# Kernel tuning notes

Measured on AMD Instinct MI355X. Metric: run time of the kernel, lower is better.

## Reference

```python
import jax, jax.numpy as jnp
import numpy as np

N_NODES = 50000
N_EDGES = 800000
N_GRAPHS = 256
NEG_SLOPE = 0.2

def selu(x):
    return jax.nn.selu(x)

def gat_conv(x, src, dst, W, att_l, att_r, b, n_nodes):
    """PyG GATConv, heads=1, with self-loops already appended to (src, dst).
    Message j->i: alpha_ij = softmax_i(leaky_relu(a_l.h_j + a_r.h_i)); out_i = sum_j alpha_ij h_j + b."""
    h = x @ W                                   # [N, C]
    a_src = h @ att_l                           # [N]
    a_dst = h @ att_r                           # [N]
    e = jax.nn.leaky_relu(a_src[src] + a_dst[dst], NEG_SLOPE)   # [E]
    # segment softmax over incoming edges of each dst node
    m = jax.ops.segment_max(e, dst, num_segments=n_nodes)       # [N]
    m = jnp.where(jnp.isfinite(m), m, 0.0)
    ex = jnp.exp(e - m[dst])
    denom = jax.ops.segment_sum(ex, dst, num_segments=n_nodes)  # [N]
    alpha = ex / jnp.maximum(denom, 1e-16)[dst]                  # [E]
    out = jax.ops.segment_sum(h[src] * alpha[:, None], dst, num_segments=n_nodes)
    return out + b

def global_mean_pool(x, batch, n_graphs):
    s = jax.ops.segment_sum(x, batch, num_segments=n_graphs)
    cnt = jax.ops.segment_sum(jnp.ones((x.shape[0],), x.dtype), batch, num_segments=n_graphs)
    return s / jnp.maximum(cnt, 1.0)[:, None]

def setup_inputs() -> dict:
    key = jax.random.key(0)
    ks = jax.random.split(key, 12)
    F_in, C, H, NC = 310, 256, 128, 2
    x = jax.random.normal(ks[0], (N_NODES, F_in), dtype=jnp.float32)
    edge_index = jax.random.randint(ks[1], (2, N_EDGES), 0, N_NODES, dtype=jnp.int64)
    batch = jnp.sort(jax.random.randint(ks[2], (N_NODES,), 0, N_GRAPHS, dtype=jnp.int64))
    g = lambda k, shp: jax.random.normal(k, shp, dtype=jnp.float32) * 0.05
    return {
        "x": x, "edge_index": edge_index, "batch": batch,
        "W1": g(ks[3], (F_in, C)), "att_l1": g(ks[4], (C,)), "att_r1": g(ks[5], (C,)),
        "b1": jnp.zeros((C,), jnp.float32),
        "W2": g(ks[6], (C, C)), "att_l2": g(ks[7], (C,)), "att_r2": g(ks[8], (C,)),
        "b2": jnp.zeros((C,), jnp.float32),
        "fc1_W": g(ks[9], (C, H)), "fc1_b": jnp.zeros((H,), jnp.float32),
        "fc2_W": g(ks[10], (H, NC)), "fc2_b": jnp.zeros((NC,), jnp.float32),
    }

def reference(x, edge_index, batch, W1, att_l1, att_r1, b1, W2, att_l2, att_r2, b2,
              fc1_W, fc1_b, fc2_W, fc2_b):
    n = x.shape[0]
    loops = jnp.arange(n, dtype=edge_index.dtype)
    src = jnp.concatenate([edge_index[0], loops])   # add_self_loops=True (PyG default)
    dst = jnp.concatenate([edge_index[1], loops])
    h = selu(gat_conv(x, src, dst, W1, att_l1, att_r1, b1, n))
    h = selu(gat_conv(h, src, dst, W2, att_l2, att_r2, b2, n))
    g = selu(global_mean_pool(h, batch, N_GRAPHS))      # [G, 256]
    g = selu(g @ fc1_W + fc1_b)                         # [G, 128]
    # dropout is identity in eval mode
    return jax.nn.log_softmax(g @ fc2_W + fc2_b, axis=-1)  # [G, 2]
```

## Files before the change

### kernel.cpp

```cpp
#include <hip/hip_runtime.h>
#include <hip/hip_bf16.h>

#define N_NODES 50000
#define N_EDGES 800000
#define N_TOT   (N_EDGES + N_NODES)
#define N_GRAPHS 256
#define F_IN 310
#define KP1 320
#define CH 256
#define HID 128
#define DEG_CAP 128

typedef __attribute__((ext_vector_type(8))) short short8;
typedef __attribute__((ext_vector_type(4))) float f32x4;
typedef unsigned short ushort_t;

__device__ __forceinline__ float selu_f(float x) {
    const float scale = 1.0507009873554805f;
    const float alpha = 1.6732632423543772f;
    return x > 0.f ? scale * x : scale * alpha * (expm1f(x));
}

__device__ __forceinline__ ushort_t f32_to_bf16_rne(float f) {
    unsigned u = __float_as_uint(f);
    unsigned rounding = 0x7FFFu + ((u >> 16) & 1u);
    return (ushort_t)((u + rounding) >> 16);
}
__device__ __forceinline__ float bf16_to_f32(ushort_t v) {
    return __uint_as_float(((unsigned)v) << 16);
}

__global__ __launch_bounds__(256) void convert_pad_x(
        const float* __restrict__ x, ushort_t* __restrict__ A) {
    int i = blockIdx.x * 256 + threadIdx.x;
    if (i >= N_NODES * (KP1 / 2)) return;
    int r = i / (KP1 / 2);
    int c2 = i - r * (KP1 / 2);
    int c = c2 * 2;
    ushort2 o = {0, 0};
    if (c2 < F_IN / 2) {
        float2 v = *(const float2*)(x + (long)r * F_IN + c);
        o.x = f32_to_bf16_rne(v.x);
        o.y = f32_to_bf16_rne(v.y);
    }
    *(ushort2*)(A + (long)r * KP1 + c) = o;
}

__global__ __launch_bounds__(256) void convert_wt_both(
        const float* __restrict__ W1, ushort_t* __restrict__ W1t,
        const float* __restrict__ W2, ushort_t* __restrict__ W2t) {
    int i = blockIdx.x * blockDim.x + threadIdx.x;
    const int n1 = CH * KP1;
    if (i < n1) {
        int n = i / KP1, k = i % KP1;
        W1t[i] = (k < F_IN) ? f32_to_bf16_rne(W1[(long)k * CH + n]) : 0;
    } else {
        int j = i - n1;
        if (j >= CH * CH) return;
        int n = j / CH, k = j % CH;
        W2t[j] = f32_to_bf16_rne(W2[(long)k * CH + n]);
    }
}

__global__ __launch_bounds__(256) void gemm_bf16_fused(
        const ushort_t* __restrict__ A, const ushort_t* __restrict__ Bt,
        ushort_t* __restrict__ Cb, const float* __restrict__ att_l,
        const float* __restrict__ att_r, float* __restrict__ a_src,
        float* __restrict__ a_dst, int M, int Kp) {
    __shared__ __align__(16) ushort_t As[2][64 * 32];
    __shared__ __align__(16) ushort_t Bs[2][256 * 32];
    __shared__ float s_pl[64], s_pr[64];
    int tid = threadIdx.x;
    int row0 = blockIdx.x * 64;
    int w = tid >> 6, l = tid & 63;
    int lr = l & 15, lc = l >> 4;
    f32x4 acc[4][4] = {};

    int srow = l >> 2;
    int sx = (l & 3) ^ (srow & 3);
    int garow = row0 + w * 16 + srow; if (garow >= M) garow = M - 1;
    const ushort_t* gA = A + (size_t)garow * Kp + sx * 8;
    const ushort_t* gB[4];
#pragma unroll
    for (int g = 0; g < 4; ++g)
        gB[g] = Bt + (size_t)(w * 64 + g * 16 + srow) * Kp + sx * 8;
    int nt = Kp >> 5;

    auto stage = [&](int sel, int k0) {
        __builtin_amdgcn_global_load_lds(
            (const __attribute__((address_space(1))) void*)(gA + k0),
            (__attribute__((address_space(3))) void*)(&As[sel][w * 16 * 32]), 16, 0, 0);
#pragma unroll
        for (int g = 0; g < 4; ++g)
            __builtin_amdgcn_global_load_lds(
                (const __attribute__((address_space(1))) void*)(gB[g] + k0),
                (__attribute__((address_space(3))) void*)(&Bs[sel][(w * 64 + g * 16) * 32]), 16, 0, 0);
    };

    stage(0, 0);
    __syncthreads();
    int cur = 0;
    for (int t = 0; t < nt; ++t) {
        if (t + 1 < nt) stage(cur ^ 1, (t + 1) << 5);
        short8 af[4], bf[4];
#pragma unroll
        for (int mi = 0; mi < 4; ++mi) {
            int r = mi * 16 + lr;
            af[mi] = *(const short8*)(&As[cur][r * 32 + ((lc ^ (r & 3)) * 8)]);
        }
#pragma unroll
        for (int ni = 0; ni < 4; ++ni) {
            int r = w * 64 + ni * 16 + lr;
            bf[ni] = *(const short8*)(&Bs[cur][r * 32 + ((lc ^ (r & 3)) * 8)]);
        }
#pragma unroll
        for (int mi = 0; mi < 4; ++mi)
#pragma unroll
            for (int ni = 0; ni < 4; ++ni)
                acc[mi][ni] = __builtin_amdgcn_mfma_f32_16x16x32_bf16(
                    af[mi], bf[ni], acc[mi][ni], 0, 0, 0);
        __syncthreads();
        cur ^= 1;
    }

    if (tid < 64) { s_pl[tid] = 0.f; s_pr[tid] = 0.f; }
    __syncthreads();
    float al[4], ar[4];
#pragma unroll
    for (int ni = 0; ni < 4; ++ni) {
        int col = w * 64 + ni * 16 + lr;
        al[ni] = att_l[col];
        ar[ni] = att_r[col];
    }
#pragma unroll
    for (int mi = 0; mi < 4; ++mi) {
        int lrow = mi * 16 + lc * 4;
#pragma unroll
        for (int q = 0; q < 4; ++q) {
            int grow = row0 + lrow + q;
            float pl = 0.f, pr = 0.f;
#pragma unroll
            for (int ni = 0; ni < 4; ++ni) {
                float v = acc[mi][ni][q];
                pl += v * al[ni];
                pr += v * ar[ni];
                if (grow < M)
                    Cb[(size_t)grow * CH + w * 64 + ni * 16 + lr] = f32_to_bf16_rne(v);
            }
#pragma unroll
            for (int off = 1; off < 16; off <<= 1) {
                pl += __shfl_xor(pl, off);
                pr += __shfl_xor(pr, off);
            }
            if (lr == 0) {
                atomicAdd(&s_pl[lrow + q], pl);
                atomicAdd(&s_pr[lrow + q], pr);
            }
        }
    }
    __syncthreads();
    if (tid < 64 && row0 + tid < M) {
        a_src[row0 + tid] = s_pl[tid];
        a_dst[row0 + tid] = s_pr[tid];
    }
}

__global__ __launch_bounds__(256) void deg_count(
        const int* __restrict__ ei, int* __restrict__ deg) {
    int eid = blockIdx.x * blockDim.x + threadIdx.x;
    if (eid >= N_TOT) return;
    int d = (eid < N_EDGES) ? ei[N_EDGES + eid] : eid - N_EDGES;
    atomicAdd(&deg[d], 1);
}

__global__ __launch_bounds__(256) void reserve_k(
        const int* __restrict__ deg, int* __restrict__ start,
        int* __restrict__ fillpos, int* __restrict__ cursor, int n) {
    int i = blockIdx.x * blockDim.x + threadIdx.x;
    if (i >= n) return;
    int s = atomicAdd(cursor, deg[i]);
    start[i] = s;
    fillpos[i] = s;
}

__global__ __launch_bounds__(256) void csr_fill(
        const int* __restrict__ ei, int* __restrict__ fillpos,
        int* __restrict__ csr_src) {
    int eid = blockIdx.x * blockDim.x + threadIdx.x;
    if (eid >= N_TOT) return;
    int s, d;
    if (eid < N_EDGES) { s = ei[eid]; d = ei[N_EDGES + eid]; }
    else { s = eid - N_EDGES; d = s; }
    int p = atomicAdd(&fillpos[d], 1);
    csr_src[p] = s;
}

__global__ __launch_bounds__(256) void gat_aggregate(
        const int* __restrict__ start, const int* __restrict__ deg,
        const int* __restrict__ csr_src,
        const float* __restrict__ a_src, const float* __restrict__ a_dst,
        const ushort_t* __restrict__ h, const float* __restrict__ bias,
        ushort_t* __restrict__ out_bf, int n) {
    __shared__ int   s_idx[4][DEG_CAP];
    __shared__ float s_ex[4][DEG_CAP];
    int wid = threadIdx.x >> 6;
    int lane = threadIdx.x & 63;
    int node = blockIdx.x * 4 + wid;
    if (node >= n) return;
    int s0 = start[node];
    int dg = deg[node];
    float ad = a_dst[node];
    bool cached = (dg <= DEG_CAP);

    float sum = 0.f;
    for (int i = lane; i < dg; i += 64) {
        int s = csr_src[s0 + i];
        float e = a_src[s] + ad;
        e = fmaxf(e, 0.2f * e);
        float ex = __expf(e);
        if (cached) { s_idx[wid][i] = s; s_ex[wid][i] = ex; }
        sum += ex;
    }
#pragma unroll
    for (int off = 32; off > 0; off >>= 1) sum += __shfl_xor(sum, off);
    float inv = 1.f / fmaxf(sum, 1e-16f);

    float4 acc = {0.f, 0.f, 0.f, 0.f};
    if (cached) {
        int i = 0;
        for (; i + 8 <= dg; i += 8) {
            int   si[8];
            float xi[8];
            ushort4 hv[8];
#pragma unroll
            for (int j = 0; j < 8; ++j) {
                si[j] = s_idx[wid][i + j];
                xi[j] = s_ex[wid][i + j] * inv;
            }
#pragma unroll
            for (int j = 0; j < 8; ++j)
                hv[j] = *(const ushort4*)(h + (long)si[j] * CH + lane * 4);
#pragma unroll
            for (int j = 0; j < 8; ++j) {
                acc.x += xi[j] * bf16_to_f32(hv[j].x);
                acc.y += xi[j] * bf16_to_f32(hv[j].y);
                acc.z += xi[j] * bf16_to_f32(hv[j].z);
                acc.w += xi[j] * bf16_to_f32(hv[j].w);
            }
        }
        for (; i + 4 <= dg; i += 4) {
            int sa = s_idx[wid][i],     sb = s_idx[wid][i + 1];
            int sc_ = s_idx[wid][i + 2], sd = s_idx[wid][i + 3];
            float xa = s_ex[wid][i] * inv,     xb = s_ex[wid][i + 1] * inv;
            float xc = s_ex[wid][i + 2] * inv, xd = s_ex[wid][i + 3] * inv;
            ushort4 ha = *(const ushort4*)(h + (long)sa * CH + lane * 4);
            ushort4 hb = *(const ushort4*)(h + (long)sb * CH + lane * 4);
            ushort4 hc = *(const ushort4*)(h + (long)sc_ * CH + lane * 4);
            ushort4 hd = *(const ushort4*)(h + (long)sd * CH + lane * 4);
            acc.x += xa * bf16_to_f32(ha.x) + xb * bf16_to_f32(hb.x)
                   + xc * bf16_to_f32(hc.x) + xd * bf16_to_f32(hd.x);
            acc.y += xa * bf16_to_f32(ha.y) + xb * bf16_to_f32(hb.y)
                   + xc * bf16_to_f32(hc.y) + xd * bf16_to_f32(hd.y);
            acc.z += xa * bf16_to_f32(ha.z) + xb * bf16_to_f32(hb.z)
                   + xc * bf16_to_f32(hc.z) + xd * bf16_to_f32(hd.z);
            acc.w += xa * bf16_to_f32(ha.w) + xb * bf16_to_f32(hb.w)
                   + xc * bf16_to_f32(hc.w) + xd * bf16_to_f32(hd.w);
        }
        for (; i < dg; i++) {
            int s = s_idx[wid][i];
            float xa = s_ex[wid][i] * inv;
            ushort4 hv = *(const ushort4*)(h + (long)s * CH + lane * 4);
            acc.x += xa * bf16_to_f32(hv.x);
            acc.y += xa * bf16_to_f32(hv.y);
            acc.z += xa * bf16_to_f32(hv.z);
            acc.w += xa * bf16_to_f32(hv.w);
        }
    } else {
        for (int i = 0; i < dg; i++) {
            int s = csr_src[s0 + i];
            float e = a_src[s] + ad;
            e = fmaxf(e, 0.2f * e);
            float alpha = __expf(e) * inv;
            ushort4 hv = *(const ushort4*)(h + (long)s * CH + lane * 4);
            acc.x += alpha * bf16_to_f32(hv.x);
            acc.y += alpha * bf16_to_f32(hv.y);
            acc.z += alpha * bf16_to_f32(hv.z);
            acc.w += alpha * bf16_to_f32(hv.w);
        }
    }
    float4 bv = *(const float4*)(bias + lane * 4);
    ushort4 ob;
    ob.x = f32_to_bf16_rne(selu_f(acc.x + bv.x));
    ob.y = f32_to_bf16_rne(selu_f(acc.y + bv.y));
    ob.z = f32_to_bf16_rne(selu_f(acc.z + bv.z));
    ob.w = f32_to_bf16_rne(selu_f(acc.w + bv.w));
    *(ushort4*)(out_bf + (long)node * CH + lane * 4) = ob;
}

__global__ __launch_bounds__(256) void pool_head_kernel(
        const ushort_t* __restrict__ h, const int* __restrict__ batch,
        const float* __restrict__ fc1W, const float* __restrict__ fc1b,
        const float* __restrict__ fc2W, const float* __restrict__ fc2b,
        float* __restrict__ out) {
    __shared__ float row[CH];
    __shared__ float hrow[HID];
    __shared__ float logits[2];
    int g = blockIdx.x;
    int t = threadIdx.x;
    int lo, hi;
    { int a = 0, b = N_NODES;
      while (a < b) { int mid = (a + b) >> 1; if (batch[mid] < g) a = mid + 1; else b = mid; }
      lo = a; }
    { int a = lo, b = N_NODES;
      while (a < b) { int mid = (a + b) >> 1; if (batch[mid] < g + 1) a = mid + 1; else b = mid; }
      hi = a; }
    float a0 = 0.f, a1 = 0.f, a2 = 0.f, a3 = 0.f;
    int i = lo;
    for (; i + 3 < hi; i += 4) {
        a0 += bf16_to_f32(h[(long)i * CH + t]);
        a1 += bf16_to_f32(h[(long)(i + 1) * CH + t]);
        a2 += bf16_to_f32(h[(long)(i + 2) * CH + t]);
        a3 += bf16_to_f32(h[(long)(i + 3) * CH + t]);
    }
    for (; i < hi; i++) a0 += bf16_to_f32(h[(long)i * CH + t]);
    float acc = (a0 + a1) + (a2 + a3);
    float cnt = (float)(hi - lo);
    row[t] = selu_f(acc / fmaxf(cnt, 1.f));
    __syncthreads();
    if (t < HID) {
        float s = fc1b[t];
        for (int k = 0; k < CH; k++) s += row[k] * fc1W[k * HID + t];
        hrow[t] = selu_f(s);
    }
    __syncthreads();
    if (t < 2) {
        float a = fc2b[t];
        for (int k = 0; k < HID; k++) a += hrow[k] * fc2W[k * 2 + t];
        logits[t] = a;
    }
    __syncthreads();
    if (t < 2) {
        float m = fmaxf(logits[0], logits[1]);
        float lse = logf(expf(logits[0] - m) + expf(logits[1] - m)) + m;
        out[g * 2 + t] = logits[t] - lse;
    }
}

extern "C" void kernel_launch(void* const* d_in, const int* in_sizes, int n_in,
                              void* d_out, int out_size, void* d_ws, size_t ws_size,
                              hipStream_t stream) {
    const float* x      = (const float*)d_in[0];
    const int*   ei     = (const int*)d_in[1];
    const int*   batch  = (const int*)d_in[2];
    const float* W1     = (const float*)d_in[3];
    const float* att_l1 = (const float*)d_in[4];
    const float* att_r1 = (const float*)d_in[5];
    const float* b1     = (const float*)d_in[6];
    const float* W2     = (const float*)d_in[7];
    const float* att_l2 = (const float*)d_in[8];
    const float* att_r2 = (const float*)d_in[9];
    const float* b2     = (const float*)d_in[10];
    const float* fc1W   = (const float*)d_in[11];
    const float* fc1b   = (const float*)d_in[12];
    const float* fc2W   = (const float*)d_in[13];
    const float* fc2b   = (const float*)d_in[14];
    float* out = (float*)d_out;

    char* ws = (char*)d_ws;
    size_t off = 0;
    auto alloc = [&](size_t bytes) {
        void* p = ws + off;
        off += (bytes + 255) & ~(size_t)255;
        return p;
    };
    ushort_t* Ab     = (ushort_t*)alloc((size_t)N_NODES * KP1 * 2);
    ushort_t* Hb1    = (ushort_t*)alloc((size_t)N_NODES * CH * 2);
    ushort_t* Zb2    = (ushort_t*)alloc((size_t)N_NODES * CH * 2);
    ushort_t* Hb2    = (ushort_t*)alloc((size_t)N_NODES * CH * 2);
    ushort_t* W1t    = (ushort_t*)alloc((size_t)CH * KP1 * 2);
    ushort_t* W2t    = (ushort_t*)alloc((size_t)CH * CH * 2);
    float*    a_src  = (float*)alloc((size_t)N_NODES * 4);
    float*    a_dst  = (float*)alloc((size_t)N_NODES * 4);
    int*      deg    = (int*)alloc((size_t)N_NODES * 4);
    int*      cursor = (int*)alloc(256);
    int*      startA = (int*)alloc((size_t)N_NODES * 4);
    int*      fillpos= (int*)alloc((size_t)N_NODES * 4);
    int*      csr_src= (int*)alloc((size_t)N_TOT * 4);

    size_t deg_pad = ((size_t)N_NODES * 4 + 255) & ~(size_t)255;

    dim3 blk(256);
    int gemm_grid = (N_NODES + 63) / 64;
    int conv_grid = (N_NODES * (KP1 / 2) + 255) / 256;
    int wt_grid   = (CH * KP1 + CH * CH + 255) / 256;
    int edge_grid = (N_TOT + 255) / 256;
    int node_grid = (N_NODES + 255) / 256;
    int agg_grid  = (N_NODES + 3) / 4;

    convert_pad_x<<<conv_grid, blk, 0, stream>>>(x, Ab);
    convert_wt_both<<<wt_grid, blk, 0, stream>>>(W1, W1t, W2, W2t);
    hipMemsetAsync(deg, 0, deg_pad + 4, stream);
    deg_count<<<edge_grid, blk, 0, stream>>>(ei, deg);
    reserve_k<<<node_grid, blk, 0, stream>>>(deg, startA, fillpos, cursor, N_NODES);
    csr_fill<<<edge_grid, blk, 0, stream>>>(ei, fillpos, csr_src);

    gemm_bf16_fused<<<gemm_grid, blk, 0, stream>>>(Ab, W1t, Hb1, att_l1, att_r1,
                                                   a_src, a_dst, N_NODES, KP1);
    gat_aggregate<<<agg_grid, blk, 0, stream>>>(startA, deg, csr_src, a_src, a_dst,
                                                Hb1, b1, Zb2, N_NODES);

    gemm_bf16_fused<<<gemm_grid, blk, 0, stream>>>(Zb2, W2t, Hb2, att_l2, att_r2,
                                                   a_src, a_dst, N_NODES, CH);
    gat_aggregate<<<agg_grid, blk, 0, stream>>>(startA, deg, csr_src, a_src, a_dst,
                                                Hb2, b2, Hb1, N_NODES);

    pool_head_kernel<<<N_GRAPHS, blk, 0, stream>>>(Hb1, batch, fc1W, fc1b,
                                                   fc2W, fc2b, out);
}
```

Before: 333.0 us.

## Fuse fp32-to-bf16 input conversion into first GEMM and widen pool head

Removes the separate convert_pad_x kernel and its padded bf16 staging buffer. The first GEMM instead loads fp32 rows of x directly, converts them to bf16 in registers, and writes them into LDS after the MFMA step, which avoids a full extra read and write pass over the input. The pooling/head kernel moves to 1024 threads, splitting the node sum across four row groups and the fc1 dot product across eight K segments, with shared-memory reductions. The trade-off is that A tiles now use register-staged synchronous loads rather than async global-to-LDS loads, so latency hiding in GEMM1 may suffer.

Result: faster. 323.4 us (-2.9%).

```diff
diff --git a/kernel.cpp b/kernel.cpp
--- a/kernel.cpp
+++ b/kernel.cpp
@@ -28,22 +28,6 @@
 }
 __device__ __forceinline__ float bf16_to_f32(ushort_t v) {
     return __uint_as_float(((unsigned)v) << 16);
-}
-
-__global__ __launch_bounds__(256) void convert_pad_x(
-        const float* __restrict__ x, ushort_t* __restrict__ A) {
-    int i = blockIdx.x * 256 + threadIdx.x;
-    if (i >= N_NODES * (KP1 / 2)) return;
-    int r = i / (KP1 / 2);
-    int c2 = i - r * (KP1 / 2);
-    int c = c2 * 2;
-    ushort2 o = {0, 0};
-    if (c2 < F_IN / 2) {
-        float2 v = *(const float2*)(x + (long)r * F_IN + c);
-        o.x = f32_to_bf16_rne(v.x);
-        o.y = f32_to_bf16_rne(v.y);
-    }
-    *(ushort2*)(A + (long)r * KP1 + c) = o;
 }
 
 __global__ __launch_bounds__(256) void convert_wt_both(
@@ -62,11 +46,12 @@
     }
 }
 
-__global__ __launch_bounds__(256) void gemm_bf16_fused(
-        const ushort_t* __restrict__ A, const ushort_t* __restrict__ Bt,
+template<int AF32>
+__global__ __launch_bounds__(256) void gemm_bf16_fused_t(
+        const void* __restrict__ Asrc, const ushort_t* __restrict__ Bt,
         ushort_t* __restrict__ Cb, const float* __restrict__ att_l,
-        const float* __restrict__ att_r, float* __restrict__ a_src,
-        float* __restrict__ a_dst, int M, int Kp) {
+        const float* __restrict__ att_r, float* __restrict__ a_srcv,
+        float* __restrict__ a_dstv, int M, int Kp) {
     __shared__ __align__(16) ushort_t As[2][64 * 32];
     __shared__ __align__(16) ushort_t Bs[2][256 * 32];
     __shared__ float s_pl[64], s_pr[64];
@@ -77,32 +62,66 @@
     f32x4 acc[4][4] = {};
 
     int srow = l >> 2;
-    int sx = (l & 3) ^ (srow & 3);
+    int sc = l & 3;
+    int sx = sc ^ (srow & 3);
     int garow = row0 + w * 16 + srow; if (garow >= M) garow = M - 1;
-    const ushort_t* gA = A + (size_t)garow * Kp + sx * 8;
     const ushort_t* gB[4];
 #pragma unroll
     for (int g = 0; g < 4; ++g)
         gB[g] = Bt + (size_t)(w * 64 + g * 16 + srow) * Kp + sx * 8;
     int nt = Kp >> 5;
 
-    auto stage = [&](int sel, int k0) {
-        __builtin_amdgcn_global_load_lds(
-            (const __attribute__((address_space(1))) void*)(gA + k0),
-            (__attribute__((address_space(3))) void*)(&As[sel][w * 16 * 32]), 16, 0, 0);
+    const ushort_t* gA = nullptr;
+    const float* xrow = nullptr;
+    if (AF32) xrow = (const float*)Asrc + (size_t)garow * F_IN;
+    else      gA = (const ushort_t*)Asrc + (size_t)garow * Kp + sx * 8;
+
+    auto stageB = [&](int sel, int k0) {
 #pragma unroll
         for (int g = 0; g < 4; ++g)
             __builtin_amdgcn_global_load_lds(
                 (const __attribute__((address_space(1))) void*)(gB[g] + k0),
                 (__attribute__((address_space(3))) void*)(&Bs[sel][(w * 64 + g * 16) * 32]), 16, 0, 0);
     };
-
-    stage(0, 0);
+    auto stageA_glds = [&](int sel, int k0) {
+        __builtin_amdgcn_global_load_lds(
+            (const __attribute__((address_space(1))) void*)(gA + k0),
+            (__attribute__((address_space(3))) void*)(&As[sel][w * 16 * 32]), 16, 0, 0);
+    };
+    float va[8];
+    auto loadA_f32 = [&](int k0) {
+        int kc = k0 + sc * 8;
+        if (kc + 8 <= F_IN) {
+#pragma unroll
+            for (int j = 0; j < 4; ++j) {
+                float2 p = *(const float2*)(xrow + kc + j * 2);
+                va[j * 2] = p.x; va[j * 2 + 1] = p.y;
+            }
+        } else {
+#pragma unroll
+            for (int j = 0; j < 8; ++j)
+                va[j] = (kc + j < F_IN) ? xrow[kc + j] : 0.f;
+        }
+    };
+    auto writeA = [&](int sel) {
+        short8 s;
+#pragma unroll
+        for (int j = 0; j < 8; ++j) s[j] = (short)f32_to_bf16_rne(va[j]);
+        *(short8*)(&As[sel][(w * 16 + srow) * 32 + sx * 8]) = s;
+    };
+
+    if (AF32) loadA_f32(0); else stageA_glds(0, 0);
+    stageB(0, 0);
+    if (AF32) writeA(0);
     __syncthreads();
     int cur = 0;
     for (int t = 0; t < nt; ++t) {
-        if (t + 1 < nt) stage(cur ^ 1, (t + 1) << 5);
-        short8 af[4], bf[4];
+        int k1 = (t + 1) << 5;
+        if (t + 1 < nt) {
+            if (AF32) loadA_f32(k1); else stageA_glds(cur ^ 1, k1);
+            stageB(cur ^ 1, k1);
+        }
+        short8 af[4], bfv[4];
 #pragma unroll
         for (int mi = 0; mi < 4; ++mi) {
             int r = mi * 16 + lr;
@@ -111,14 +130,15 @@
 #pragma unroll
         for (int ni = 0; ni < 4; ++ni) {
             int r = w * 64 + ni * 16 + lr;
-            bf[ni] = *(const short8*)(&Bs[cur][r * 32 + ((lc ^ (r & 3)) * 8)]);
+            bfv[ni] = *(const short8*)(&Bs[cur][r * 32 + ((lc ^ (r & 3)) * 8)]);
         }
 #pragma unroll
         for (int mi = 0; mi < 4; ++mi)
 #pragma unroll
             for (int ni = 0; ni < 4; ++ni)
                 acc[mi][ni] = __builtin_amdgcn_mfma_f32_16x16x32_bf16(
-                    af[mi], bf[ni], acc[mi][ni], 0, 0, 0);
+                    af[mi], bfv[ni], acc[mi][ni], 0, 0, 0);
+        if (AF32 && t + 1 < nt) writeA(cur ^ 1);
         __syncthreads();
         cur ^= 1;
     }
@@ -160,8 +180,8 @@
     }
     __syncthreads();
     if (tid < 64 && row0 + tid < M) {
-        a_src[row0 + tid] = s_pl[tid];
-        a_dst[row0 + tid] = s_pr[tid];
+        a_srcv[row0 + tid] = s_pl[tid];
+        a_dstv[row0 + tid] = s_pr[tid];
     }
 }
 
@@ -297,16 +317,20 @@
     *(ushort4*)(out_bf + (long)node * CH + lane * 4) = ob;
 }
 
-__global__ __launch_bounds__(256) void pool_head_kernel(
+__global__ __launch_bounds__(1024) void pool_head_kernel(
         const ushort_t* __restrict__ h, const int* __restrict__ batch,
         const float* __restrict__ fc1W, const float* __restrict__ fc1b,
         const float* __restrict__ fc2W, const float* __restrict__ fc2b,
         float* __restrict__ out) {
+    __shared__ float part[4][CH];
     __shared__ float row[CH];
+    __shared__ float part2[8][HID];
     __shared__ float hrow[HID];
     __shared__ float logits[2];
     int g = blockIdx.x;
-    int t = threadIdx.x;
+    int tid = threadIdx.x;
+    int t = tid & 255;
+    int quad = tid >> 8;
     int lo, hi;
     { int a = 0, b = N_NODES;
       while (a < b) { int mid = (a + b) >> 1; if (batch[mid] < g) a = mid + 1; else b = mid; }
@@ -314,35 +338,47 @@
     { int a = lo, b = N_NODES;
       while (a < b) { int mid = (a + b) >> 1; if (batch[mid] < g + 1) a = mid + 1; else b = mid; }
       hi = a; }
-    float a0 = 0.f, a1 = 0.f, a2 = 0.f, a3 = 0.f;
-    int i = lo;
-    for (; i + 3 < hi; i += 4) {
+    float a0 = 0.f, a1 = 0.f;
+    int i = lo + quad;
+    for (; i + 4 < hi; i += 8) {
         a0 += bf16_to_f32(h[(long)i * CH + t]);
-        a1 += bf16_to_f32(h[(long)(i + 1) * CH + t]);
-        a2 += bf16_to_f32(h[(long)(i + 2) * CH + t]);
-        a3 += bf16_to_f32(h[(long)(i + 3) * CH + t]);
-    }
-    for (; i < hi; i++) a0 += bf16_to_f32(h[(long)i * CH + t]);
-    float acc = (a0 + a1) + (a2 + a3);
-    float cnt = (float)(hi - lo);
-    row[t] = selu_f(acc / fmaxf(cnt, 1.f));
-    __syncthreads();
-    if (t < HID) {
-        float s = fc1b[t];
-        for (int k = 0; k < CH; k++) s += row[k] * fc1W[k * HID + t];
-        hrow[t] = selu_f(s);
-    }
-    __syncthreads();
-    if (t < 2) {
-        float a = fc2b[t];
-        for (int k = 0; k < HID; k++) a += hrow[k] * fc2W[k * 2 + t];
-        logits[t] = a;
-    }
-    __syncthreads();
-    if (t < 2) {
+        a1 += bf16_to_f32(h[(long)(i + 4) * CH + t]);
+    }
+    for (; i < hi; i += 4) a0 += bf16_to_f32(h[(long)i * CH + t]);
+    part[quad][t] = a0 + a1;
+    __syncthreads();
+    if (quad == 0) {
+        float cnt = (float)(hi - lo);
+        float acc = (part[0][t] + part[1][t]) + (part[2][t] + part[3][t]);
+        row[t] = selu_f(acc / fmaxf(cnt, 1.f));
+    }
+    __syncthreads();
+    {
+        int o = tid & 127;
+        int seg = tid >> 7;
+        float s = 0.f;
+        int k0 = seg * 32;
+        for (int k = k0; k < k0 + 32; ++k) s += row[k] * fc1W[k * HID + o];
+        part2[seg][o] = s;
+    }
+    __syncthreads();
+    if (tid < HID) {
+        float s = fc1b[tid];
+#pragma unroll
+        for (int j = 0; j < 8; ++j) s += part2[j][tid];
+        hrow[tid] = selu_f(s);
+    }
+    __syncthreads();
+    if (tid < 2) {
+        float a = fc2b[tid];
+        for (int k = 0; k < HID; k++) a += hrow[k] * fc2W[k * 2 + tid];
+        logits[tid] = a;
+    }
+    __syncthreads();
+    if (tid < 2) {
         float m = fmaxf(logits[0], logits[1]);
         float lse = logf(expf(logits[0] - m) + expf(logits[1] - m)) + m;
-        out[g * 2 + t] = logits[t] - lse;
+        out[g * 2 + tid] = logits[tid] - lse;
     }
 }
 
@@ -373,7 +409,6 @@
         off += (bytes + 255) & ~(size_t)255;
         return p;
     };
-    ushort_t* Ab     = (ushort_t*)alloc((size_t)N_NODES * KP1 * 2);
     ushort_t* Hb1    = (ushort_t*)alloc((size_t)N_NODES * CH * 2);
     ushort_t* Zb2    = (ushort_t*)alloc((size_t)N_NODES * CH * 2);
     ushort_t* Hb2    = (ushort_t*)alloc((size_t)N_NODES * CH * 2);
@@ -391,29 +426,27 @@
 
     dim3 blk(256);
     int gemm_grid = (N_NODES + 63) / 64;
-    int conv_grid = (N_NODES * (KP1 / 2) + 255) / 256;
     int wt_grid   = (CH * KP1 + CH * CH + 255) / 256;
     int edge_grid = (N_TOT + 255) / 256;
     int node_grid = (N_NODES + 255) / 256;
     int agg_grid  = (N_NODES + 3) / 4;
 
-    convert_pad_x<<<conv_grid, blk, 0, stream>>>(x, Ab);
     convert_wt_both<<<wt_grid, blk, 0, stream>>>(W1, W1t, W2, W2t);
     hipMemsetAsync(deg, 0, deg_pad + 4, stream);
     deg_count<<<edge_grid, blk, 0, stream>>>(ei, deg);
     reserve_k<<<node_grid, blk, 0, stream>>>(deg, startA, fillpos, cursor, N_NODES);
     csr_fill<<<edge_grid, blk, 0, stream>>>(ei, fillpos, csr_src);
 
-    gemm_bf16_fused<<<gemm_grid, blk, 0, stream>>>(Ab, W1t, Hb1, att_l1, att_r1,
-                                                   a_src, a_dst, N_NODES, KP1);
+    gemm_bf16_fused_t<1><<<gemm_grid, blk, 0, stream>>>(x, W1t, Hb1, att_l1, att_r1,
+                                                        a_src, a_dst, N_NODES, KP1);
     gat_aggregate<<<agg_grid, blk, 0, stream>>>(startA, deg, csr_src, a_src, a_dst,
                                                 Hb1, b1, Zb2, N_NODES);
 
-    gemm_bf16_fused<<<gemm_grid, blk, 0, stream>>>(Zb2, W2t, Hb2, att_l2, att_r2,
-                                                   a_src, a_dst, N_NODES, CH);
+    gemm_bf16_fused_t<0><<<gemm_grid, blk, 0, stream>>>(Zb2, W2t, Hb2, att_l2, att_r2,
+                                                        a_src, a_dst, N_NODES, CH);
     gat_aggregate<<<agg_grid, blk, 0, stream>>>(startA, deg, csr_src, a_src, a_dst,
                                                 Hb2, b2, Hb1, N_NODES);
 
-    pool_head_kernel<<<N_GRAPHS, blk, 0, stream>>>(Hb1, batch, fc1W, fc1b,
-                                                   fc2W, fc2b, out);
-}
+    pool_head_kernel<<<N_GRAPHS, dim3(1024), 0, stream>>>(Hb1, batch, fc1W, fc1b,
+                                                          fc2W, fc2b, out);
+}
```
